# Kernel tuning notes

Measured on AMD Instinct MI355X. Metric: run time of the kernel, lower is better.

The kernel has to match this reference:

```python
import jax, jax.numpy as jnp
import numpy as np

EMB = 64
L = 2
NU = 100000
NI = 50000
ER = 1000000
ET = 800000
EP = 200000


def setup_inputs() -> dict:
    key = jax.random.key(0)
    ks = jax.random.split(key, 32)
    f = jnp.float32
    def nrm(k, shape, s=0.01):
        return (jax.random.normal(k, shape) * s).astype(f)
    inp = {}
    # graph structure (int)
    inp['rate_src'] = jax.random.randint(ks[0], (ER,), 0, NU)
    inp['rate_dst'] = jax.random.randint(ks[1], (ER,), 0, NI)
    inp['trust_src'] = jax.random.randint(ks[2], (ET,), 0, NU)
    inp['trust_dst'] = jax.random.randint(ks[3], (ET,), 0, NU)
    inp['pos_u'] = jax.random.randint(ks[4], (EP,), 0, NU)
    inp['pos_i'] = jax.random.randint(ks[5], (EP,), 0, NI)
    inp['neg_u'] = jax.random.randint(ks[6], (EP,), 0, NU)
    inp['neg_i'] = jax.random.randint(ks[7], (EP,), 0, NI)
    # embeddings (init normal(0, 0.01) per init_weights)
    inp['eu'] = nrm(ks[8], (NU, EMB))
    inp['ei'] = nrm(ks[9], (NI, EMB))
    # per-rel GATv2 params, stacked over L layers; [:,0]=fc_src, [:,1]=fc_dst
    inp['rate_W'] = nrm(ks[10], (L, 2, EMB, EMB))
    inp['rate_b'] = jnp.zeros((L, 2, EMB), f)
    inp['rate_attn'] = nrm(ks[11], (L, EMB), 0.1)
    inp['rate_bias'] = jnp.zeros((L, EMB), f)
    inp['rb_W'] = nrm(ks[12], (L, 2, EMB, EMB))
    inp['rb_b'] = jnp.zeros((L, 2, EMB), f)
    inp['rb_attn'] = nrm(ks[13], (L, EMB), 0.1)
    inp['rb_bias'] = jnp.zeros((L, EMB), f)
    inp['tr_W'] = nrm(ks[14], (L, 2, EMB, EMB))
    inp['tr_b'] = jnp.zeros((L, 2, EMB), f)
    inp['tr_attn'] = nrm(ks[15], (L, EMB), 0.1)
    inp['tr_bias'] = jnp.zeros((L, EMB), f)
    # attention-gate MLPs: [:, 0]=influence, [:, 1]=interest
    inp['attW1'] = nrm(ks[16], (L, 2, 2 * EMB, 2 * EMB))
    inp['attb1'] = jnp.zeros((L, 2, 2 * EMB), f)
    inp['attW2'] = nrm(ks[17], (L, 2, 2 * EMB))
    inp['attb2'] = jnp.zeros((L, 2), f)
    return inp


def gatv2(hs, hd, src, dst, Ws, bs, Wd, bd, attn, bias, n_dst):
    # DGL GATv2Conv, num_heads=1: e = attn . leaky_relu(Ws h_u + Wd h_v), slope 0.2
    fs = hs @ Ws + bs          # [Ns, E]
    fd = hd @ Wd + bd          # [Nd, E]
    e = jax.nn.leaky_relu(fs[src] + fd[dst], 0.2) @ attn  # [E]
    m = jax.ops.segment_max(e, dst, num_segments=n_dst)
    ex = jnp.exp(e - m[dst])
    denom = jax.ops.segment_sum(ex, dst, num_segments=n_dst)
    alpha = ex / denom[dst]
    out = jax.ops.segment_sum(alpha[:, None] * fs[src], dst, num_segments=n_dst)
    return out + bias


def _bn1(x):
    # BatchNorm1d(1), training-mode batch stats, affine identity at init
    mu = jnp.mean(x)
    var = jnp.mean((x - mu) ** 2)
    return (x - mu) * jax.lax.rsqrt(var + 1e-5)


def reference(eu, ei, rate_W, rate_b, rate_attn, rate_bias, rb_W, rb_b, rb_attn,
              rb_bias, tr_W, tr_b, tr_attn, tr_bias, attW1, attb1, attW2, attb2,
              rate_src, rate_dst, trust_src, trust_dst, pos_u, pos_i, neg_u, neg_i):
    n_users, n_items = eu.shape[0], ei.shape[0]
    hu, hi = eu, ei
    res_u, res_i = [eu], [ei]
    for l in range(rate_W.shape[0]):
        # interest diffusion: rate (user->item) and rated-by (item->user, reverse edges)
        hi_new = gatv2(hu, hi, rate_src, rate_dst, rate_W[l, 0], rate_b[l, 0],
                       rate_W[l, 1], rate_b[l, 1], rate_attn[l], rate_bias[l], n_items) + hi
        q = gatv2(hi, hu, rate_dst, rate_src, rb_W[l, 0], rb_b[l, 0],
                  rb_W[l, 1], rb_b[l, 1], rb_attn[l], rb_bias[l], n_users)
        # influence diffusion: trust (user->user)
        p = gatv2(hu, hu, trust_src, trust_dst, tr_W[l, 0], tr_b[l, 0],
                  tr_W[l, 1], tr_b[l, 1], tr_attn[l], tr_bias[l], n_users)
        def att(h2, i):
            z = (h2 @ attW1[l, i] + attb1[l, i]) @ attW2[l, i] + attb2[l, i]  # [N]
            return jax.nn.leaky_relu(_bn1(z), 0.01)
        a_inf = att(jnp.concatenate([hu, p], axis=1), 0)
        a_int = att(jnp.concatenate([hu, q], axis=1), 1)
        gamma = jax.nn.softmax(jnp.stack([a_inf, a_int], axis=1), axis=1)  # [N,2]
        hu = gamma[:, 0:1] * p + gamma[:, 1:2] * q + hu
        hi = hi_new
        res_u.append(hu)
        res_i.append(hi)
    hu_all = jnp.concatenate(res_u, axis=1)  # [NU, EMB*(1+L)]
    hi_all = jnp.concatenate(res_i, axis=1)
    pos = jnp.sum(hu_all[pos_u] * hi_all[pos_i], axis=1, keepdims=True)  # [EP,1]
    neg = jnp.sum(hu_all[neg_u] * hi_all[neg_i], axis=1, keepdims=True)
    return pos, neg
```

## Files before the change

kernel.cpp:

```cpp
#include <hip/hip_runtime.h>
#include <hip/hip_bf16.h>
#include <hip/hip_fp16.h>
#include <cstdint>

typedef __hip_bfloat16 bf16;
typedef __attribute__((ext_vector_type(8))) short frag_ab;
typedef __attribute__((ext_vector_type(4))) float frag_cd;
typedef __attribute__((ext_vector_type(4))) short short4v;
typedef __attribute__((ext_vector_type(8))) short short8v;
typedef unsigned short u16;

#define CAPA 56
#define CAPB 40
#define CAPC 32

__device__ __forceinline__ float b2f(short s){
  return __uint_as_float(((unsigned)(unsigned short)s) << 16);
}
__device__ __forceinline__ float h2f(short s){
  __half h; __builtin_memcpy(&h, &s, 2); return __half2float(h);
}
__device__ __forceinline__ short f2h_s(float x){
  __half h = __float2half(x);
  short s; __builtin_memcpy(&s, &h, 2); return s;
}
__device__ __forceinline__ void bf_split(float x, short& hi, short& lo){
  bf16 h = __float2bfloat16(x);
  float hf = __bfloat162float(h);
  bf16 l = __float2bfloat16(x - hf);
  __builtin_memcpy(&hi, &h, 2);
  __builtin_memcpy(&lo, &l, 2);
}

__device__ __forceinline__ float wave_sum(float v){
#pragma unroll
  for (int o = 32; o > 0; o >>= 1) v += __shfl_down(v, o, 64);
  return v;
}

__global__ void k_wsplit(const float* __restrict__ rateW, const float* __restrict__ rbW,
                         const float* __restrict__ trW,
                         short* __restrict__ Whi, short* __restrict__ Wlo){
  int tid = blockIdx.x * 256 + threadIdx.x;
  if (tid >= 12 * 4096) return;
  int m = tid >> 12, rem = tid & 4095;
  int lane = rem >> 6, rem2 = rem & 63;
  int pair = rem2 >> 3, j = rem2 & 7;
  int c = pair >> 1, h = pair & 1;
  int rel = m >> 2, li = m & 3;
  const float* base = (rel == 0) ? rateW : (rel == 1) ? rbW : trW;
  float v = base[(size_t)li * 4096 + (32 * h + (lane >> 4) * 8 + j) * 64 + 16 * c + (lane & 15)];
  short sh, sl; bf_split(v, sh, sl);
  Whi[tid] = sh; Wlo[tid] = sl;
}

__device__ __forceinline__ void dev_linear(int rowb, int nloc, int gofs, int nglob,
    const float* __restrict__ x, int xs, int xo,
    const short* __restrict__ Whi, const short* __restrict__ Wlo, int mcount,
    int m0, int m1, int m2, int m3,
    const float* b0, const float* b1, const float* b2, const float* b3,
    bf16* o0, bf16* o1, bf16* o2, bf16* o3){
  int lane = threadIdx.x & 63, w = threadIdx.x >> 6;
  int quad = lane >> 4, n16 = lane & 15;
  int rowbase = rowb + w * 16;
  if (rowbase >= nloc) return;
  int lrow = rowbase + n16; if (lrow >= nloc) lrow = nloc - 1;
  const float* xp = x + (size_t)lrow * xs + xo;
  frag_ab ahi[2], alo[2];
#pragma unroll
  for (int h = 0; h < 2; ++h){
    frag_ab vh, vl;
#pragma unroll
    for (int j = 0; j < 8; ++j){
      float xv = xp[32 * h + quad * 8 + j];
      short sh, sl; bf_split(xv, sh, sl);
      vh[j] = sh; vl[j] = sl;
    }
    ahi[h] = vh; alo[h] = vl;
  }
  int ms[4] = {m0, m1, m2, m3};
  const float* bs[4] = {b0, b1, b2, b3};
  bf16* os[4] = {o0, o1, o2, o3};
  for (int i = 0; i < mcount; ++i){
    const frag_ab* Bh = (const frag_ab*)(Whi + (size_t)ms[i] * 4096 + lane * 64);
    const frag_ab* Bl = (const frag_ab*)(Wlo + (size_t)ms[i] * 4096 + lane * 64);
    frag_cd acc[4];
#pragma unroll
    for (int c = 0; c < 4; ++c) acc[c] = frag_cd{0.f, 0.f, 0.f, 0.f};
#pragma unroll
    for (int c = 0; c < 4; ++c)
#pragma unroll
      for (int h = 0; h < 2; ++h){
        frag_ab bh = Bh[c * 2 + h], bl = Bl[c * 2 + h];
        acc[c] = __builtin_amdgcn_mfma_f32_16x16x32_bf16(ahi[h], bh, acc[c], 0, 0, 0);
        acc[c] = __builtin_amdgcn_mfma_f32_16x16x32_bf16(alo[h], bh, acc[c], 0, 0, 0);
        acc[c] = __builtin_amdgcn_mfma_f32_16x16x32_bf16(ahi[h], bl, acc[c], 0, 0, 0);
      }
    const float* bb = bs[i];
    bf16* oo = os[i];
#pragma unroll
    for (int reg = 0; reg < 4; ++reg){
      int r = rowbase + quad * 4 + reg;
      if (r >= nloc || gofs + r >= nglob) continue;
#pragma unroll
      for (int c = 0; c < 4; ++c)
        oo[(size_t)(gofs + r) * 64 + 16 * c + n16] = __float2bfloat16(acc[c][reg] + bb[16 * c + n16]);
    }
  }
}

struct LinArgs {
  int nblk; const float* x; int xs, xo, n, mcount;
  int m0, m1, m2, m3;
  const float *b0, *b1, *b2, *b3;
  bf16 *o0, *o1, *o2, *o3;
};
struct PrepArgs {
  int NBH, NBC, ER, ET, NU, NI;
  const int *rate_src, *rate_dst, *trust_dst;
  int *cntA, *cntB, *cntC;
  u16 *posA, *posB, *posC;
  const float *eu, *ei;
  float *hu01, *hi01;
  const short *Whi, *Wlo;
  LinArgs LU, LI;
  const float *W1, *b1v, *W2, *b2v;
  float *vvec, *cs;
};

__global__ void k_prep(PrepArgs a){
  int b = blockIdx.x, t = threadIdx.x;
  if (b < a.NBH){
    int k = b * 256 + t;
    if (k < a.ER){
      int d = a.rate_dst[k], s = a.rate_src[k];
      a.posA[k] = (u16)atomicAdd(a.cntA + d, 1);
      a.posB[k] = (u16)atomicAdd(a.cntB + s, 1);
    }
    if (k < a.ET){
      a.posC[k] = (u16)atomicAdd(a.cntC + a.trust_dst[k], 1);
    }
    return;
  }
  b -= a.NBH;
  if (b < a.LU.nblk){
    dev_linear(b * 64, a.LU.n, 0, a.LU.n, a.LU.x, a.LU.xs, a.LU.xo, a.Whi, a.Wlo,
               a.LU.mcount, a.LU.m0, a.LU.m1, a.LU.m2, a.LU.m3,
               a.LU.b0, a.LU.b1, a.LU.b2, a.LU.b3, a.LU.o0, a.LU.o1, a.LU.o2, a.LU.o3);
    return;
  }
  b -= a.LU.nblk;
  if (b < a.LI.nblk){
    dev_linear(b * 64, a.LI.n, 0, a.LI.n, a.LI.x, a.LI.xs, a.LI.xo, a.Whi, a.Wlo,
               a.LI.mcount, a.LI.m0, a.LI.m1, a.LI.m2, a.LI.m3,
               a.LI.b0, a.LI.b1, a.LI.b2, a.LI.b3, a.LI.o0, a.LI.o1, a.LI.o2, a.LI.o3);
    return;
  }
  b -= a.LI.nblk;
  if (b < a.NBC){
    int tot = (a.NU + a.NI) * 16;
    int tu = a.NU * 16;
    int base = b * 1024 + t;
#pragma unroll
    for (int s = 0; s < 4; ++s){
      int idx = base + s * 256;
      if (idx >= tot) break;
      if (idx < tu){
        int r = idx >> 4, jj = idx & 15;
        *(float4*)(a.hu01 + (size_t)r * 128 + 4 * jj) =
            *(const float4*)(a.eu + (size_t)r * 64 + 4 * jj);
      } else {
        int t2 = idx - tu;
        int r = t2 >> 4, jj = t2 & 15;
        *(float4*)(a.hi01 + (size_t)r * 128 + 4 * jj) =
            *(const float4*)(a.ei + (size_t)r * 64 + 4 * jj);
      }
    }
    return;
  }
  for (int it = t; it < 512; it += 256){
    int li = it >> 7, r = it & 127;
    float acc = 0.f;
    for (int c = 0; c < 128; ++c)
      acc += a.W1[(size_t)(li * 128 + r) * 128 + c] * a.W2[li * 128 + c];
    a.vvec[li * 128 + r] = acc;
    if (r == 0){
      float cacc = a.b2v[li];
      for (int c = 0; c < 128; ++c)
        cacc += a.b1v[li * 128 + c] * a.W2[li * 128 + c];
      a.cs[li] = cacc;
    }
  }
}

__global__ void k_fill(const int* __restrict__ rs_, const int* __restrict__ rd_,
                       const int* __restrict__ ts_, const int* __restrict__ td_,
                       const u16* __restrict__ posA, const u16* __restrict__ posB,
                       const u16* __restrict__ posC,
                       int* __restrict__ csrA, u16* __restrict__ csrB,
                       int* __restrict__ csrC, int ER, int ET){
  int k = blockIdx.x * 256 + threadIdx.x;
  if (k < ER){
    int s = rs_[k], d = rd_[k];
    int pa = posA[k], pb = posB[k];
    if (pa < CAPA) csrA[(size_t)d * CAPA + pa] = s;
    if (pb < CAPB) csrB[(size_t)s * CAPB + pb] = (u16)d;
  }
  if (k < ET){
    int pc = posC[k];
    if (pc < CAPC) csrC[(size_t)td_[k] * CAPC + pc] = ts_[k];
  }
}

struct GatArgs {
  int nblk, n, of16;
  const int *cnt;
  const int *csr; const u16 *csr16;
  const bf16 *fs, *fd;
  const float *attn, *bias;
  void *out; int os, oo;
  const float *res; int rs, ro;
};

template<int CAP>
__device__ __forceinline__ void dev_gat(int lb, const GatArgs& g){
  int d = lb * 4 + (threadIdx.x >> 6);
  if (d >= g.n) return;
  int lane = threadIdx.x & 63;
  int gg = lane >> 3, l8 = lane & 7;
  int c = g.cnt[d]; if (c > CAP) c = CAP;
  size_t base = (size_t)d * CAP;
  int my_s = 0;
  if (lane < c) my_s = g.csr16 ? (int)g.csr16[base + lane] : g.csr[base + lane];
  short8v dv = *(const short8v*)(g.fd + (size_t)d * 64 + 8 * l8);
  float fdv[8];
#pragma unroll
  for (int j = 0; j < 8; ++j) fdv[j] = b2f(dv[j]);
  float4 a0 = *(const float4*)(g.attn + 8 * l8);
  float4 a1 = *(const float4*)(g.attn + 8 * l8 + 4);
  float a8[8] = {a0.x, a0.y, a0.z, a0.w, a1.x, a1.y, a1.z, a1.w};
  constexpr int NIT = CAP / 8;
  short8v rows[NIT];
#pragma unroll
  for (int it = 0; it < NIT; ++it){
    if (it * 8 < c){
      int e = it * 8 + gg;
      int s = __shfl(my_s, (e < c) ? e : it * 8, 64);
      rows[it] = *(const short8v*)(g.fs + (size_t)s * 64 + 8 * l8);
    }
  }
  float acc[8];
#pragma unroll
  for (int j = 0; j < 8; ++j) acc[j] = 0.f;
  float den = 0.f;
#pragma unroll
  for (int it = 0; it < NIT; ++it){
    if (it * 8 < c){
      bool valid = (it * 8 + gg) < c;
      float f[8];
      float tt = 0.f;
#pragma unroll
      for (int j = 0; j < 8; ++j){
        f[j] = b2f(rows[it][j]);
        float v = f[j] + fdv[j];
        v = (v > 0.f) ? v : 0.2f * v;
        tt += v * a8[j];
      }
#pragma unroll
      for (int o = 1; o < 8; o <<= 1) tt += __shfl_xor(tt, o, 64);
      float ex = valid ? __expf(tt) : 0.f;
#pragma unroll
      for (int j = 0; j < 8; ++j) acc[j] += ex * f[j];
      den += ex;
    }
  }
#pragma unroll
  for (int o = 8; o < 64; o <<= 1){
#pragma unroll
    for (int j = 0; j < 8; ++j) acc[j] += __shfl_xor(acc[j], o, 64);
    den += __shfl_xor(den, o, 64);
  }
  if (gg == 0){
    float inv = (den > 0.f) ? 1.f / den : 0.f;
    float4 b0 = *(const float4*)(g.bias + 8 * l8);
    float4 b1 = *(const float4*)(g.bias + 8 * l8 + 4);
    float o8[8];
    o8[0] = acc[0] * inv + b0.x; o8[1] = acc[1] * inv + b0.y;
    o8[2] = acc[2] * inv + b0.z; o8[3] = acc[3] * inv + b0.w;
    o8[4] = acc[4] * inv + b1.x; o8[5] = acc[5] * inv + b1.y;
    o8[6] = acc[6] * inv + b1.z; o8[7] = acc[7] * inv + b1.w;
    if (g.res){
      float4 r0 = *(const float4*)(g.res + (size_t)d * g.rs + g.ro + 8 * l8);
      float4 r1 = *(const float4*)(g.res + (size_t)d * g.rs + g.ro + 8 * l8 + 4);
      o8[0] += r0.x; o8[1] += r0.y; o8[2] += r0.z; o8[3] += r0.w;
      o8[4] += r1.x; o8[5] += r1.y; o8[6] += r1.z; o8[7] += r1.w;
    }
    if (g.of16){
      short8v hv;
#pragma unroll
      for (int j = 0; j < 8; ++j) hv[j] = f2h_s(o8[j]);
      *(short8v*)((short*)g.out + (size_t)d * g.os + g.oo + 8 * l8) = hv;
    } else {
      float* op = (float*)g.out + (size_t)d * g.os + g.oo + 8 * l8;
      *(float4*)op = make_float4(o8[0], o8[1], o8[2], o8[3]);
      *(float4*)(op + 4) = make_float4(o8[4], o8[5], o8[6], o8[7]);
    }
  }
}

template<int CA, int CB, int CC>
__global__ void k_gat3(GatArgs A, GatArgs B, GatArgs C){
  int b = blockIdx.x;
  if (b < A.nblk){ dev_gat<CA>(b, A); return; }
  b -= A.nblk;
  if (b < B.nblk){ dev_gat<CB>(b, B); return; }
  b -= B.nblk;
  dev_gat<CC>(b, C);
}

struct GzArgs {
  int nbz, NU, l;
  const float* hu01;
  const __half* pf16;
  const __half* q;
  const float *vvec, *cs;
  float *z1, *z2, *bsums;
  const short *Whi, *Wlo;
  LinArgs LI;
};

__global__ void k_gatez(GzArgs a){
  int b = blockIdx.x;
  if (b >= a.nbz){
    int blk = b - a.nbz;
    dev_linear(blk * 64, a.LI.n, 0, a.LI.n, a.LI.x, a.LI.xs, a.LI.xo, a.Whi, a.Wlo,
               a.LI.mcount, a.LI.m0, a.LI.m1, a.LI.m2, a.LI.m3,
               a.LI.b0, a.LI.b1, a.LI.b2, a.LI.b3, a.LI.o0, a.LI.o1, a.LI.o2, a.LI.o3);
    return;
  }
  __shared__ float part[4][4];
  int w = threadIdx.x >> 6, j = threadIdx.x & 63;
  int nidx = b * 4 + w;
  float lz1 = 0.f, lz2 = 0.f;
  if (nidx < a.NU){
    const float* v1 = a.vvec + a.l * 256;
    const float* v2 = a.vvec + a.l * 256 + 128;
    float h  = a.hu01[(size_t)nidx * 128 + a.l * 64 + j];
    float pv = a.pf16 ? h2f(((const short*)a.pf16)[(size_t)nidx * 64 + j])
                      : a.hu01[(size_t)nidx * 128 + 64 + j];
    float qv = h2f(((const short*)a.q)[(size_t)nidx * 64 + j]);
    float t1 = wave_sum(h * v1[j] + pv * v1[64 + j]);
    float t2 = wave_sum(h * v2[j] + qv * v2[64 + j]);
    if (j == 0){
      lz1 = t1 + a.cs[a.l * 2 + 0];
      lz2 = t2 + a.cs[a.l * 2 + 1];
      a.z1[nidx] = lz1;
      a.z2[nidx] = lz2;
    }
  }
  if (j == 0){
    part[w][0] = lz1; part[w][1] = lz1 * lz1;
    part[w][2] = lz2; part[w][3] = lz2 * lz2;
  }
  __syncthreads();
  if (threadIdx.x < 4)
    a.bsums[(size_t)b * 4 + threadIdx.x] =
        part[0][threadIdx.x] + part[1][threadIdx.x] +
        part[2][threadIdx.x] + part[3][threadIdx.x];
}

__global__ void k_bn(const float* __restrict__ bsums, int nb,
                     double* __restrict__ gpart, double* __restrict__ sums,
                     int* __restrict__ tick){
  __shared__ double sh[256];
  __shared__ int lastflag;
  int c = threadIdx.x & 3, r0 = blockIdx.x * 64 + (threadIdx.x >> 2);
  double acc = 0.0;
  for (int i = r0; i < nb; i += gridDim.x * 64)
    acc += (double)bsums[(size_t)i * 4 + c];
  sh[threadIdx.x] = acc;
  __syncthreads();
  for (int s = 128; s >= 4; s >>= 1){
    if (threadIdx.x < s) sh[threadIdx.x] += sh[threadIdx.x + s];
    __syncthreads();
  }
  if (threadIdx.x < 4) gpart[(size_t)blockIdx.x * 4 + threadIdx.x] = sh[threadIdx.x];
  __threadfence();
  if (threadIdx.x == 0) lastflag = (atomicAdd(tick, 1) == (int)gridDim.x - 1);
  __syncthreads();
  if (lastflag){
    __threadfence();
    int k0 = threadIdx.x >> 2;
    double a2 = 0.0;
    for (int i = k0; i < (int)gridDim.x; i += 64) a2 += gpart[(size_t)i * 4 + c];
    sh[threadIdx.x] = a2;
    __syncthreads();
    for (int s = 128; s >= 4; s >>= 1){
      if (threadIdx.x < s) sh[threadIdx.x] += sh[threadIdx.x + s];
      __syncthreads();
    }
    if (threadIdx.x < 4) sums[threadIdx.x] = sh[threadIdx.x];
  }
}

struct CmbArgs {
  int l, NU;
  float* hu01; __half* hu2; const __half* q;
  const float *z1, *z2; const double* sums;
  int dolin;
  const short *Whi, *Wlo;
  int m0, m1, m2, m3;
  const float *b0, *b1, *b2, *b3;
  bf16 *o0, *o1, *o2, *o3;
};

__global__ void k_combine(CmbArgs a){
  __shared__ float lds[64][65];
  int r0 = blockIdx.x * 64;
  int t = threadIdx.x;
  double invn = 1.0 / (double)a.NU;
  double mu1 = a.sums[0] * invn, mu2 = a.sums[2] * invn;
  float var1 = (float)(a.sums[1] * invn - mu1 * mu1);
  float var2 = (float)(a.sums[3] * invn - mu2 * mu2);
  float rs1 = rsqrtf(var1 + 1e-5f), rs2 = rsqrtf(var2 + 1e-5f);
  int nloc = a.NU - r0; if (nloc > 64) nloc = 64;
#pragma unroll
  for (int s = 0; s < 16; ++s){
    int elem = s * 256 + t;
    int row = elem >> 6, col = elem & 63;
    if (row < nloc){
      int r = r0 + row;
      float a1 = (a.z1[r] - (float)mu1) * rs1;
      float a2 = (a.z2[r] - (float)mu2) * rs2;
      a1 = a1 > 0.f ? a1 : 0.01f * a1;
      a2 = a2 > 0.f ? a2 : 0.01f * a2;
      float mx = fmaxf(a1, a2);
      float e1 = __expf(a1 - mx), e2 = __expf(a2 - mx);
      float inv = 1.f / (e1 + e2);
      float pv = (a.l == 0) ? a.hu01[(size_t)r * 128 + 64 + col]
                            : h2f(((const short*)a.hu2)[(size_t)r * 64 + col]);
      float qv = h2f(((const short*)a.q)[(size_t)r * 64 + col]);
      float h  = a.hu01[(size_t)r * 128 + a.l * 64 + col];
      float out = e1 * inv * pv + e2 * inv * qv + h;
      if (a.l == 0){
        a.hu01[(size_t)r * 128 + 64 + col] = out;
        lds[row][col] = out;
      } else {
        ((short*)a.hu2)[(size_t)r * 64 + col] = f2h_s(out);
      }
    }
  }
  if (!a.dolin) return;
  __syncthreads();
  dev_linear(0, nloc, r0, a.NU, &lds[0][0], 65, 0, a.Whi, a.Wlo, 4,
             a.m0, a.m1, a.m2, a.m3, a.b0, a.b1, a.b2, a.b3,
             a.o0, a.o1, a.o2, a.o3);
}

__global__ void k_score(const int* __restrict__ pu, const int* __restrict__ pi,
                        const int* __restrict__ nu, const int* __restrict__ ni,
                        const float* __restrict__ hu01, const __half* __restrict__ hu2,
                        const float* __restrict__ hi01, const __half* __restrict__ hi2,
                        float* __restrict__ out, int EP){
  int gw = blockIdx.x * 4 + (threadIdx.x >> 6);
  int sub = (threadIdx.x >> 4) & 3, l16 = threadIdx.x & 15;
  int k = gw * 4 + sub;
  if (k >= 2 * EP) return;
  int u, i;
  if (k < EP){ u = pu[k]; i = pi[k]; } else { u = nu[k - EP]; i = ni[k - EP]; }
  const float4* A = (const float4*)(hu01 + (size_t)u * 128);
  const float4* B = (const float4*)(hi01 + (size_t)i * 128);
  float acc = 0.f;
#pragma unroll
  for (int t = 0; t < 2; ++t){
    float4 av = A[l16 + 16 * t];
    float4 bv = B[l16 + 16 * t];
    acc += av.x * bv.x + av.y * bv.y + av.z * bv.z + av.w * bv.w;
  }
  short4v ha = *(const short4v*)((const short*)hu2 + (size_t)u * 64 + 4 * l16);
  short4v hb = *(const short4v*)((const short*)hi2 + (size_t)i * 64 + 4 * l16);
  acc += h2f(ha[0]) * h2f(hb[0]) + h2f(ha[1]) * h2f(hb[1])
       + h2f(ha[2]) * h2f(hb[2]) + h2f(ha[3]) * h2f(hb[3]);
#pragma unroll
  for (int o = 8; o > 0; o >>= 1) acc += __shfl_xor(acc, o, 64);
  if (l16 == 0) out[k] = acc;
}

extern "C" void kernel_launch(void* const* d_in, const int* in_sizes, int n_in,
                              void* d_out, int out_size, void* d_ws, size_t ws_size,
                              hipStream_t stream) {
  const int*   rate_src  = (const int*)  d_in[0];
  const int*   rate_dst  = (const int*)  d_in[1];
  const int*   trust_src = (const int*)  d_in[2];
  const int*   trust_dst = (const int*)  d_in[3];
  const int*   pos_u     = (const int*)  d_in[4];
  const int*   pos_i     = (const int*)  d_in[5];
  const int*   neg_u     = (const int*)  d_in[6];
  const int*   neg_i     = (const int*)  d_in[7];
  const float* eu        = (const float*)d_in[8];
  const float* ei        = (const float*)d_in[9];
  const float* rate_W    = (const float*)d_in[10];
  const float* rate_b    = (const float*)d_in[11];
  const float* rate_attn = (const float*)d_in[12];
  const float* rate_bias = (const float*)d_in[13];
  const float* rb_W      = (const float*)d_in[14];
  const float* rb_b      = (const float*)d_in[15];
  const float* rb_attn   = (const float*)d_in[16];
  const float* rb_bias   = (const float*)d_in[17];
  const float* tr_W      = (const float*)d_in[18];
  const float* tr_b      = (const float*)d_in[19];
  const float* tr_attn   = (const float*)d_in[20];
  const float* tr_bias   = (const float*)d_in[21];
  const float* attW1     = (const float*)d_in[22];
  const float* attb1     = (const float*)d_in[23];
  const float* attW2     = (const float*)d_in[24];
  const float* attb2     = (const float*)d_in[25];

  const int ER = in_sizes[0];
  const int ET = in_sizes[2];
  const int EP = in_sizes[4];
  const int NU = in_sizes[8] / 64;
  const int NI = in_sizes[9] / 64;
  const int EM = (ER > ET) ? ER : ET;

  float*  wsp    = (float*)d_ws;
  float*  hu01   = wsp;
  float*  hi01   = hu01 + (size_t)NU * 128;
  __half* hi2    = (__half*)(hi01 + (size_t)NI * 128);
  __half* hu2    = hi2 + (size_t)NI * 64;
  __half* qf     = hu2 + (size_t)NU * 64;
  u16*    posA   = (u16*)qf;
  u16*    posB   = posA + ER;
  u16*    posC   = posB + ER;
  bf16*   fdA    = (bf16*)(qf + (size_t)NU * 64);
  bf16*   fsB    = fdA + (size_t)NI * 64;
  bf16*   tb     = fsB + (size_t)NI * 64;
  bf16*   fsA    = tb;
  bf16*   fdB    = tb + (size_t)NU * 64;
  bf16*   fsC    = tb + (size_t)NU * 128;
  bf16*   fdC    = tb + (size_t)NU * 192;
  float*  z1     = (float*)(tb + (size_t)NU * 256);
  float*  z2     = z1 + NU;
  float*  bsums  = z2 + NU;
  float*  vvec   = bsums + (size_t)(((NU + 3) / 4) * 4);
  float*  cs     = vvec + 512;
  double* sums   = (double*)(((uintptr_t)(cs + 4) + 15) & ~(uintptr_t)15);
  double* gpart  = sums + 4;
  short*  Whi    = (short*)(gpart + 512);
  short*  Wlo    = Whi + 12 * 4096;
  int*    cntA   = (int*)(Wlo + 12 * 4096);
  int*    cntB   = cntA + NI;
  int*    cntC   = cntB + NU;
  int*    tick   = cntC + NU;
  int*    csrA   = tick + 8;
  u16*    csrB   = (u16*)(csrA + (size_t)NI * CAPA);
  int*    csrC   = (int*)(csrB + (size_t)NU * CAPB);

  auto cdiv = [](int a, int b){ return (a + b - 1) / b; };
  const int nbz = cdiv(NU, 4);

  hipMemsetAsync(cntA, 0, (size_t)(NI + 2 * NU + 8) * 4, stream);
  k_wsplit<<<192, 256, 0, stream>>>(rate_W, rb_W, tr_W, Whi, Wlo);

  PrepArgs pa;
  pa.NBH = cdiv(EM, 256);
  pa.NBC = cdiv((NU + NI) * 16, 1024);
  pa.ER = ER; pa.ET = ET; pa.NU = NU; pa.NI = NI;
  pa.rate_src = rate_src; pa.rate_dst = rate_dst; pa.trust_dst = trust_dst;
  pa.cntA = cntA; pa.cntB = cntB; pa.cntC = cntC;
  pa.posA = posA; pa.posB = posB; pa.posC = posC;
  pa.eu = eu; pa.ei = ei; pa.hu01 = hu01; pa.hi01 = hi01;
  pa.Whi = Whi; pa.Wlo = Wlo;
  pa.LU.nblk = cdiv(NU, 64); pa.LU.x = eu; pa.LU.xs = 64; pa.LU.xo = 0;
  pa.LU.n = NU; pa.LU.mcount = 4;
  pa.LU.m0 = 0; pa.LU.m1 = 5; pa.LU.m2 = 8; pa.LU.m3 = 9;
  pa.LU.b0 = rate_b + 0;  pa.LU.b1 = rb_b + 64;
  pa.LU.b2 = tr_b + 0;    pa.LU.b3 = tr_b + 64;
  pa.LU.o0 = fsA; pa.LU.o1 = fdB; pa.LU.o2 = fsC; pa.LU.o3 = fdC;
  pa.LI.nblk = cdiv(NI, 64); pa.LI.x = ei; pa.LI.xs = 64; pa.LI.xo = 0;
  pa.LI.n = NI; pa.LI.mcount = 2;
  pa.LI.m0 = 1; pa.LI.m1 = 4; pa.LI.m2 = 0; pa.LI.m3 = 0;
  pa.LI.b0 = rate_b + 64; pa.LI.b1 = rb_b + 0;
  pa.LI.b2 = nullptr; pa.LI.b3 = nullptr;
  pa.LI.o0 = fdA; pa.LI.o1 = fsB; pa.LI.o2 = nullptr; pa.LI.o3 = nullptr;
  pa.W1 = attW1; pa.b1v = attb1; pa.W2 = attW2; pa.b2v = attb2;
  pa.vvec = vvec; pa.cs = cs;
  k_prep<<<pa.NBH + pa.LU.nblk + pa.LI.nblk + pa.NBC + 1, 256, 0, stream>>>(pa);

  k_fill<<<cdiv(EM, 256), 256, 0, stream>>>(rate_src, rate_dst, trust_src, trust_dst,
      posA, posB, posC, csrA, csrB, csrC, ER, ET);

  for (int l = 0; l < 2; ++l){
    GatArgs A, B, C;
    A.nblk = cdiv(NI, 4); A.n = NI;
    A.cnt = cntA; A.csr = csrA; A.csr16 = nullptr; A.fs = fsA; A.fd = fdA;
    A.attn = rate_attn + l * 64; A.bias = rate_bias + l * 64;
    if (l == 0){ A.of16 = 0; A.out = hi01; A.os = 128; A.oo = 64;
                 A.res = hi01; A.rs = 128; A.ro = 0; }
    else       { A.of16 = 1; A.out = hi2;  A.os = 64;  A.oo = 0;
                 A.res = hi01; A.rs = 128; A.ro = 64; }
    B.nblk = cdiv(NU, 4); B.n = NU; B.of16 = 1;
    B.cnt = cntB; B.csr = nullptr; B.csr16 = csrB; B.fs = fsB; B.fd = fdB;
    B.attn = rb_attn + l * 64; B.bias = rb_bias + l * 64;
    B.out = qf; B.os = 64; B.oo = 0;
    B.res = nullptr; B.rs = 0; B.ro = 0;
    C.nblk = cdiv(NU, 4); C.n = NU;
    C.cnt = cntC; C.csr = csrC; C.csr16 = nullptr; C.fs = fsC; C.fd = fdC;
    C.attn = tr_attn + l * 64; C.bias = tr_bias + l * 64;
    if (l == 0){ C.of16 = 0; C.out = hu01; C.os = 128; C.oo = 64; }
    else       { C.of16 = 1; C.out = hu2;  C.os = 64;  C.oo = 0;  }
    C.res = nullptr; C.rs = 0; C.ro = 0;
    k_gat3<CAPA, CAPB, CAPC><<<A.nblk + B.nblk + C.nblk, 256, 0, stream>>>(A, B, C);

    GzArgs gz;
    gz.nbz = nbz; gz.NU = NU; gz.l = l;
    gz.hu01 = hu01; gz.pf16 = (l == 0) ? nullptr : hu2; gz.q = qf;
    gz.vvec = vvec; gz.cs = cs; gz.z1 = z1; gz.z2 = z2; gz.bsums = bsums;
    gz.Whi = Whi; gz.Wlo = Wlo;
    if (l == 0){
      gz.LI.nblk = cdiv(NI, 64); gz.LI.x = hi01; gz.LI.xs = 128; gz.LI.xo = 64;
      gz.LI.n = NI; gz.LI.mcount = 2;
      gz.LI.m0 = 3; gz.LI.m1 = 6; gz.LI.m2 = 0; gz.LI.m3 = 0;
      gz.LI.b0 = rate_b + 192; gz.LI.b1 = rb_b + 128;
      gz.LI.b2 = nullptr; gz.LI.b3 = nullptr;
      gz.LI.o0 = fdA; gz.LI.o1 = fsB; gz.LI.o2 = nullptr; gz.LI.o3 = nullptr;
    } else {
      gz.LI.nblk = 0; gz.LI.x = nullptr; gz.LI.xs = 0; gz.LI.xo = 0;
      gz.LI.n = 0; gz.LI.mcount = 0;
      gz.LI.m0 = gz.LI.m1 = gz.LI.m2 = gz.LI.m3 = 0;
      gz.LI.b0 = gz.LI.b1 = gz.LI.b2 = gz.LI.b3 = nullptr;
      gz.LI.o0 = gz.LI.o1 = gz.LI.o2 = gz.LI.o3 = nullptr;
    }
    k_gatez<<<nbz + gz.LI.nblk, 256, 0, stream>>>(gz);

    k_bn<<<128, 256, 0, stream>>>(bsums, nbz, gpart, sums, tick + l);

    CmbArgs cm;
    cm.l = l; cm.NU = NU;
    cm.hu01 = hu01; cm.hu2 = hu2; cm.q = qf;
    cm.z1 = z1; cm.z2 = z2; cm.sums = sums;
    cm.dolin = (l == 0) ? 1 : 0;
    cm.Whi = Whi; cm.Wlo = Wlo;
    cm.m0 = 2; cm.m1 = 7; cm.m2 = 10; cm.m3 = 11;
    cm.b0 = rate_b + 128; cm.b1 = rb_b + 192;
    cm.b2 = tr_b + 128;   cm.b3 = tr_b + 192;
    cm.o0 = fsA; cm.o1 = fdB; cm.o2 = fsC; cm.o3 = fdC;
    k_combine<<<cdiv(NU, 64), 256, 0, stream>>>(cm);
  }

  k_score<<<cdiv(2 * EP, 16), 256, 0, stream>>>(pos_u, pos_i, neg_u, neg_i,
      hu01, hu2, hi01, hi2, (float*)d_out, EP);
}
```

Measured before the change: 913.3 us.

## Drop embedding copy into interleaved buffers and software-pipeline GAT neighbor loads

Layer-0 features are now read straight from the input embeddings, replacing the interleaved 128-wide hu01/hi01 buffers with separate 64-wide p1/hi1 buffers. This removes the copy pass in the prep kernel and narrows row strides. The GAT gather loop changes from fully unrolled per-CAP register arrays to a runtime loop that keeps two rows prefetched ahead. That should lower register pressure and skip iterations past the edge count, but it exposes less memory-level parallelism per wave. The gatez kernel also reorders its blocks so the linear-layer blocks come first.

```diff
diff --git a/kernel.cpp b/kernel.cpp
--- a/kernel.cpp
+++ b/kernel.cpp
@@ -116,12 +116,10 @@
   bf16 *o0, *o1, *o2, *o3;
 };
 struct PrepArgs {
-  int NBH, NBC, ER, ET, NU, NI;
+  int NBH, ER, ET;
   const int *rate_src, *rate_dst, *trust_dst;
   int *cntA, *cntB, *cntC;
   u16 *posA, *posB, *posC;
-  const float *eu, *ei;
-  float *hu01, *hi01;
   const short *Whi, *Wlo;
   LinArgs LU, LI;
   const float *W1, *b1v, *W2, *b2v;
@@ -154,28 +152,6 @@
     dev_linear(b * 64, a.LI.n, 0, a.LI.n, a.LI.x, a.LI.xs, a.LI.xo, a.Whi, a.Wlo,
                a.LI.mcount, a.LI.m0, a.LI.m1, a.LI.m2, a.LI.m3,
                a.LI.b0, a.LI.b1, a.LI.b2, a.LI.b3, a.LI.o0, a.LI.o1, a.LI.o2, a.LI.o3);
-    return;
-  }
-  b -= a.LI.nblk;
-  if (b < a.NBC){
-    int tot = (a.NU + a.NI) * 16;
-    int tu = a.NU * 16;
-    int base = b * 1024 + t;
-#pragma unroll
-    for (int s = 0; s < 4; ++s){
-      int idx = base + s * 256;
-      if (idx >= tot) break;
-      if (idx < tu){
-        int r = idx >> 4, jj = idx & 15;
-        *(float4*)(a.hu01 + (size_t)r * 128 + 4 * jj) =
-            *(const float4*)(a.eu + (size_t)r * 64 + 4 * jj);
-      } else {
-        int t2 = idx - tu;
-        int r = t2 >> 4, jj = t2 & 15;
-        *(float4*)(a.hi01 + (size_t)r * 128 + 4 * jj) =
-            *(const float4*)(a.ei + (size_t)r * 64 + 4 * jj);
-      }
-    }
     return;
   }
   for (int it = t; it < 512; it += 256){
@@ -239,40 +215,47 @@
   float4 a0 = *(const float4*)(g.attn + 8 * l8);
   float4 a1 = *(const float4*)(g.attn + 8 * l8 + 4);
   float a8[8] = {a0.x, a0.y, a0.z, a0.w, a1.x, a1.y, a1.z, a1.w};
-  constexpr int NIT = CAP / 8;
-  short8v rows[NIT];
-#pragma unroll
-  for (int it = 0; it < NIT; ++it){
-    if (it * 8 < c){
-      int e = it * 8 + gg;
-      int s = __shfl(my_s, (e < c) ? e : it * 8, 64);
-      rows[it] = *(const short8v*)(g.fs + (size_t)s * 64 + 8 * l8);
-    }
-  }
   float acc[8];
 #pragma unroll
   for (int j = 0; j < 8; ++j) acc[j] = 0.f;
   float den = 0.f;
-#pragma unroll
-  for (int it = 0; it < NIT; ++it){
-    if (it * 8 < c){
-      bool valid = (it * 8 + gg) < c;
-      float f[8];
-      float tt = 0.f;
-#pragma unroll
-      for (int j = 0; j < 8; ++j){
-        f[j] = b2f(rows[it][j]);
-        float v = f[j] + fdv[j];
-        v = (v > 0.f) ? v : 0.2f * v;
-        tt += v * a8[j];
-      }
-#pragma unroll
-      for (int o = 1; o < 8; o <<= 1) tt += __shfl_xor(tt, o, 64);
-      float ex = valid ? __expf(tt) : 0.f;
-#pragma unroll
-      for (int j = 0; j < 8; ++j) acc[j] += ex * f[j];
-      den += ex;
-    }
+  short8v s0, s1;
+  {
+    int e = gg;
+    int ss = __shfl(my_s, (e < c) ? e : 0, 64);
+    s0 = *(const short8v*)(g.fs + (size_t)ss * 64 + 8 * l8);
+  }
+  s1 = s0;
+  if (8 < c){
+    int e = 8 + gg;
+    int ss = __shfl(my_s, (e < c) ? e : 8, 64);
+    s1 = *(const short8v*)(g.fs + (size_t)ss * 64 + 8 * l8);
+  }
+  for (int idx = 0; idx < c; idx += 8){
+    short8v cur = s0;
+    s0 = s1;
+    int nn = idx + 16;
+    if (nn < c){
+      int e = nn + gg;
+      int ss = __shfl(my_s, (e < c) ? e : nn, 64);
+      s1 = *(const short8v*)(g.fs + (size_t)ss * 64 + 8 * l8);
+    }
+    bool valid = (idx + gg) < c;
+    float f[8];
+    float tt = 0.f;
+#pragma unroll
+    for (int j = 0; j < 8; ++j){
+      f[j] = b2f(cur[j]);
+      float v = f[j] + fdv[j];
+      v = (v > 0.f) ? v : 0.2f * v;
+      tt += v * a8[j];
+    }
+#pragma unroll
+    for (int o = 1; o < 8; o <<= 1) tt += __shfl_xor(tt, o, 64);
+    float ex = valid ? __expf(tt) : 0.f;
+#pragma unroll
+    for (int j = 0; j < 8; ++j) acc[j] += ex * f[j];
+    den += ex;
   }
 #pragma unroll
   for (int o = 8; o < 64; o <<= 1){
@@ -320,7 +303,8 @@
 
 struct GzArgs {
   int nbz, NU, l;
-  const float* hu01;
+  const float* hptr;
+  const float* pf32;
   const __half* pf16;
   const __half* q;
   const float *vvec, *cs;
@@ -331,13 +315,13 @@
 
 __global__ void k_gatez(GzArgs a){
   int b = blockIdx.x;
-  if (b >= a.nbz){
-    int blk = b - a.nbz;
-    dev_linear(blk * 64, a.LI.n, 0, a.LI.n, a.LI.x, a.LI.xs, a.LI.xo, a.Whi, a.Wlo,
+  if (b < a.LI.nblk){
+    dev_linear(b * 64, a.LI.n, 0, a.LI.n, a.LI.x, a.LI.xs, a.LI.xo, a.Whi, a.Wlo,
                a.LI.mcount, a.LI.m0, a.LI.m1, a.LI.m2, a.LI.m3,
                a.LI.b0, a.LI.b1, a.LI.b2, a.LI.b3, a.LI.o0, a.LI.o1, a.LI.o2, a.LI.o3);
     return;
   }
+  b -= a.LI.nblk;
   __shared__ float part[4][4];
   int w = threadIdx.x >> 6, j = threadIdx.x & 63;
   int nidx = b * 4 + w;
@@ -345,9 +329,9 @@
   if (nidx < a.NU){
     const float* v1 = a.vvec + a.l * 256;
     const float* v2 = a.vvec + a.l * 256 + 128;
-    float h  = a.hu01[(size_t)nidx * 128 + a.l * 64 + j];
+    float h  = a.hptr[(size_t)nidx * 64 + j];
     float pv = a.pf16 ? h2f(((const short*)a.pf16)[(size_t)nidx * 64 + j])
-                      : a.hu01[(size_t)nidx * 128 + 64 + j];
+                      : a.pf32[(size_t)nidx * 64 + j];
     float qv = h2f(((const short*)a.q)[(size_t)nidx * 64 + j]);
     float t1 = wave_sum(h * v1[j] + pv * v1[64 + j]);
     float t2 = wave_sum(h * v2[j] + qv * v2[64 + j]);
@@ -405,7 +389,8 @@
 
 struct CmbArgs {
   int l, NU;
-  float* hu01; __half* hu2; const __half* q;
+  const float* hptr;
+  float* p1; __half* hu2; const __half* q;
   const float *z1, *z2; const double* sums;
   int dolin;
   const short *Whi, *Wlo;
@@ -437,13 +422,13 @@
       float mx = fmaxf(a1, a2);
       float e1 = __expf(a1 - mx), e2 = __expf(a2 - mx);
       float inv = 1.f / (e1 + e2);
-      float pv = (a.l == 0) ? a.hu01[(size_t)r * 128 + 64 + col]
+      float pv = (a.l == 0) ? a.p1[(size_t)r * 64 + col]
                             : h2f(((const short*)a.hu2)[(size_t)r * 64 + col]);
       float qv = h2f(((const short*)a.q)[(size_t)r * 64 + col]);
-      float h  = a.hu01[(size_t)r * 128 + a.l * 64 + col];
+      float h  = a.hptr[(size_t)r * 64 + col];
       float out = e1 * inv * pv + e2 * inv * qv + h;
       if (a.l == 0){
-        a.hu01[(size_t)r * 128 + 64 + col] = out;
+        a.p1[(size_t)r * 64 + col] = out;
         lds[row][col] = out;
       } else {
         ((short*)a.hu2)[(size_t)r * 64 + col] = f2h_s(out);
@@ -459,8 +444,10 @@
 
 __global__ void k_score(const int* __restrict__ pu, const int* __restrict__ pi,
                         const int* __restrict__ nu, const int* __restrict__ ni,
-                        const float* __restrict__ hu01, const __half* __restrict__ hu2,
-                        const float* __restrict__ hi01, const __half* __restrict__ hi2,
+                        const float* __restrict__ eu, const float* __restrict__ p1,
+                        const __half* __restrict__ hu2,
+                        const float* __restrict__ ei, const float* __restrict__ hi1,
+                        const __half* __restrict__ hi2,
                         float* __restrict__ out, int EP){
   int gw = blockIdx.x * 4 + (threadIdx.x >> 6);
   int sub = (threadIdx.x >> 4) & 3, l16 = threadIdx.x & 15;
@@ -468,15 +455,12 @@
   if (k >= 2 * EP) return;
   int u, i;
   if (k < EP){ u = pu[k]; i = pi[k]; } else { u = nu[k - EP]; i = ni[k - EP]; }
-  const float4* A = (const float4*)(hu01 + (size_t)u * 128);
-  const float4* B = (const float4*)(hi01 + (size_t)i * 128);
-  float acc = 0.f;
-#pragma unroll
-  for (int t = 0; t < 2; ++t){
-    float4 av = A[l16 + 16 * t];
-    float4 bv = B[l16 + 16 * t];
-    acc += av.x * bv.x + av.y * bv.y + av.z * bv.z + av.w * bv.w;
-  }
+  float4 a0 = *(const float4*)(eu + (size_t)u * 64 + 4 * l16);
+  float4 b0 = *(const float4*)(ei + (size_t)i * 64 + 4 * l16);
+  float4 a1 = *(const float4*)(p1 + (size_t)u * 64 + 4 * l16);
+  float4 b1 = *(const float4*)(hi1 + (size_t)i * 64 + 4 * l16);
+  float acc = a0.x * b0.x + a0.y * b0.y + a0.z * b0.z + a0.w * b0.w
+            + a1.x * b1.x + a1.y * b1.y + a1.z * b1.z + a1.w * b1.w;
   short4v ha = *(const short4v*)((const short*)hu2 + (size_t)u * 64 + 4 * l16);
   short4v hb = *(const short4v*)((const short*)hi2 + (size_t)i * 64 + 4 * l16);
   acc += h2f(ha[0]) * h2f(hb[0]) + h2f(ha[1]) * h2f(hb[1])
@@ -524,11 +508,11 @@
   const int EM = (ER > ET) ? ER : ET;
 
   float*  wsp    = (float*)d_ws;
-  float*  hu01   = wsp;
-  float*  hi01   = hu01 + (size_t)NU * 128;
-  __half* hi2    = (__half*)(hi01 + (size_t)NI * 128);
-  __half* hu2    = hi2 + (size_t)NI * 64;
-  __half* qf     = hu2 + (size_t)NU * 64;
+  float*  p1     = wsp;
+  float*  hi1    = p1 + (size_t)NU * 64;
+  __half* hu2    = (__half*)(hi1 + (size_t)NI * 64);
+  __half* hi2    = hu2 + (size_t)NU * 64;
+  __half* qf     = hi2 + (size_t)NI * 64;
   u16*    posA   = (u16*)qf;
   u16*    posB   = posA + ER;
   u16*    posC   = posB + ER;
@@ -564,12 +548,10 @@
 
   PrepArgs pa;
   pa.NBH = cdiv(EM, 256);
-  pa.NBC = cdiv((NU + NI) * 16, 1024);
-  pa.ER = ER; pa.ET = ET; pa.NU = NU; pa.NI = NI;
+  pa.ER = ER; pa.ET = ET;
   pa.rate_src = rate_src; pa.rate_dst = rate_dst; pa.trust_dst = trust_dst;
   pa.cntA = cntA; pa.cntB = cntB; pa.cntC = cntC;
   pa.posA = posA; pa.posB = posB; pa.posC = posC;
-  pa.eu = eu; pa.ei = ei; pa.hu01 = hu01; pa.hi01 = hi01;
   pa.Whi = Whi; pa.Wlo = Wlo;
   pa.LU.nblk = cdiv(NU, 64); pa.LU.x = eu; pa.LU.xs = 64; pa.LU.xo = 0;
   pa.LU.n = NU; pa.LU.mcount = 4;
@@ -585,7 +567,7 @@
   pa.LI.o0 = fdA; pa.LI.o1 = fsB; pa.LI.o2 = nullptr; pa.LI.o3 = nullptr;
   pa.W1 = attW1; pa.b1v = attb1; pa.W2 = attW2; pa.b2v = attb2;
   pa.vvec = vvec; pa.cs = cs;
-  k_prep<<<pa.NBH + pa.LU.nblk + pa.LI.nblk + pa.NBC + 1, 256, 0, stream>>>(pa);
+  k_prep<<<pa.NBH + pa.LU.nblk + pa.LI.nblk + 1, 256, 0, stream>>>(pa);
 
   k_fill<<<cdiv(EM, 256), 256, 0, stream>>>(rate_src, rate_dst, trust_src, trust_dst,
       posA, posB, posC, csrA, csrB, csrC, ER, ET);
@@ -595,10 +577,10 @@
     A.nblk = cdiv(NI, 4); A.n = NI;
     A.cnt = cntA; A.csr = csrA; A.csr16 = nullptr; A.fs = fsA; A.fd = fdA;
     A.attn = rate_attn + l * 64; A.bias = rate_bias + l * 64;
-    if (l == 0){ A.of16 = 0; A.out = hi01; A.os = 128; A.oo = 64;
-                 A.res = hi01; A.rs = 128; A.ro = 0; }
-    else       { A.of16 = 1; A.out = hi2;  A.os = 64;  A.oo = 0;
-                 A.res = hi01; A.rs = 128; A.ro = 64; }
+    if (l == 0){ A.of16 = 0; A.out = hi1; A.os = 64; A.oo = 0;
+                 A.res = ei;  A.rs = 64; A.ro = 0; }
+    else       { A.of16 = 1; A.out = hi2; A.os = 64; A.oo = 0;
+                 A.res = hi1; A.rs = 64; A.ro = 0; }
     B.nblk = cdiv(NU, 4); B.n = NU; B.of16 = 1;
     B.cnt = cntB; B.csr = nullptr; B.csr16 = csrB; B.fs = fsB; B.fd = fdB;
     B.attn = rb_attn + l * 64; B.bias = rb_bias + l * 64;
@@ -607,18 +589,21 @@
     C.nblk = cdiv(NU, 4); C.n = NU;
     C.cnt = cntC; C.csr = csrC; C.csr16 = nullptr; C.fs = fsC; C.fd = fdC;
     C.attn = tr_attn + l * 64; C.bias = tr_bias + l * 64;
-    if (l == 0){ C.of16 = 0; C.out = hu01; C.os = 128; C.oo = 64; }
-    else       { C.of16 = 1; C.out = hu2;  C.os = 64;  C.oo = 0;  }
+    if (l == 0){ C.of16 = 0; C.out = p1;  C.os = 64; C.oo = 0; }
+    else       { C.of16 = 1; C.out = hu2; C.os = 64; C.oo = 0; }
     C.res = nullptr; C.rs = 0; C.ro = 0;
     k_gat3<CAPA, CAPB, CAPC><<<A.nblk + B.nblk + C.nblk, 256, 0, stream>>>(A, B, C);
 
     GzArgs gz;
     gz.nbz = nbz; gz.NU = NU; gz.l = l;
-    gz.hu01 = hu01; gz.pf16 = (l == 0) ? nullptr : hu2; gz.q = qf;
+    gz.hptr = (l == 0) ? eu : p1;
+    gz.pf32 = p1;
+    gz.pf16 = (l == 0) ? (const __half*)nullptr : hu2;
+    gz.q = qf;
     gz.vvec = vvec; gz.cs = cs; gz.z1 = z1; gz.z2 = z2; gz.bsums = bsums;
     gz.Whi = Whi; gz.Wlo = Wlo;
     if (l == 0){
-      gz.LI.nblk = cdiv(NI, 64); gz.LI.x = hi01; gz.LI.xs = 128; gz.LI.xo = 64;
+      gz.LI.nblk = cdiv(NI, 64); gz.LI.x = hi1; gz.LI.xs = 64; gz.LI.xo = 0;
       gz.LI.n = NI; gz.LI.mcount = 2;
       gz.LI.m0 = 3; gz.LI.m1 = 6; gz.LI.m2 = 0; gz.LI.m3 = 0;
       gz.LI.b0 = rate_b + 192; gz.LI.b1 = rb_b + 128;
@@ -637,7 +622,8 @@
 
     CmbArgs cm;
     cm.l = l; cm.NU = NU;
-    cm.hu01 = hu01; cm.hu2 = hu2; cm.q = qf;
+    cm.hptr = (l == 0) ? eu : p1;
+    cm.p1 = p1; cm.hu2 = hu2; cm.q = qf;
     cm.z1 = z1; cm.z2 = z2; cm.sums = sums;
     cm.dolin = (l == 0) ? 1 : 0;
     cm.Whi = Whi; cm.Wlo = Wlo;
@@ -649,5 +635,5 @@
   }
 
   k_score<<<cdiv(2 * EP, 16), 256, 0, stream>>>(pos_u, pos_i, neg_u, neg_i,
-      hu01, hu2, hi01, hi2, (float*)d_out, EP);
-}
+      eu, p1, hu2, ei, hi1, hi2, (float*)d_out, EP);
+}
```

Result: faster. 892.7 us (-2.3%).
